# Optimization experiments

Hardware: AMD Instinct MI355X
Metric: run time of the kernel (lower is better)

Reference implementation:

```python
import jax, jax.numpy as jnp
import numpy as np

EMBED_DIM = 1024
NUM_HEADS = 16
HEAD_DIM = EMBED_DIM // NUM_HEADS
SCALE = 1.0 / np.sqrt(HEAD_DIM)


def _quant_linear(x, w, b):
    # Per-tensor symmetric int8 quantize -> dequantize -> GEMM (faithful to QuantizedLinear)
    s = jnp.max(jnp.abs(w)) / 127.0
    w_dq = jnp.clip(jnp.round(w / s), -128.0, 127.0) * s
    return jnp.einsum('bse,oe->bso', x, w_dq) + b


def setup_inputs() -> dict:
    key = jax.random.key(0)
    ks = jax.random.split(key, 7)
    B, S, E = 2, 2048, EMBED_DIM
    return {
        'query': jax.random.normal(ks[0], (B, S, E), dtype=jnp.float32),
        'key': jax.random.normal(ks[1], (B, S, E), dtype=jnp.float32),
        'value': jax.random.normal(ks[2], (B, S, E), dtype=jnp.float32),
        'Wq': jax.random.normal(ks[3], (E, E), dtype=jnp.float32) * 0.02,
        'bq': jnp.zeros((E,), dtype=jnp.float32),
        'Wk': jax.random.normal(ks[4], (E, E), dtype=jnp.float32) * 0.02,
        'bk': jnp.zeros((E,), dtype=jnp.float32),
        'Wv': jax.random.normal(ks[5], (E, E), dtype=jnp.float32) * 0.02,
        'bv': jnp.zeros((E,), dtype=jnp.float32),
        'Wo': jax.random.normal(ks[6], (E, E), dtype=jnp.float32) * 0.02,
        'bo': jnp.zeros((E,), dtype=jnp.float32),
    }


def reference(query, key, value, Wq, bq, Wk, bk, Wv, bv, Wo, bo):
    B, S, E = query.shape
    H, D = NUM_HEADS, HEAD_DIM
    Q = _quant_linear(query, Wq, bq).reshape(B, S, H, D).transpose(0, 2, 1, 3)
    K = _quant_linear(key, Wk, bk).reshape(B, S, H, D).transpose(0, 2, 1, 3)
    V = _quant_linear(value, Wv, bv).reshape(B, S, H, D).transpose(0, 2, 1, 3)
    # [B,H,S,S] unfused attention scores
    scores = jnp.einsum('bhqd,bhkd->bhqk', Q, K) * SCALE
    attn = jax.nn.softmax(scores, axis=-1)  # dropout is identity at inference
    out = jnp.einsum('bhqk,bhkd->bhqd', attn, V)
    out = out.transpose(0, 2, 1, 3).reshape(B, S, E)
    return _quant_linear(out, Wo, bo)
```

## Files before the change

### kernel.cpp

```cpp
#include <hip/hip_runtime.h>
#include <math.h>

#define S_LEN 2048
#define EMB   1024
#define NHEAD 16
#define HDIM  64
#define MTOT  4096
#define EXP2_SCALE 0.18033688011112042f

typedef __attribute__((ext_vector_type(8))) short bf16x8;
typedef __attribute__((ext_vector_type(4))) float f32x4;

__device__ __forceinline__ short f2bf(float f) {
  union { float f; unsigned u; } v; v.f = f;
  unsigned r = v.u + 0x7fffu + ((v.u >> 16) & 1u);
  return (short)(r >> 16);
}
__device__ __forceinline__ float bf2f(short s) {
  union { float f; unsigned u; } v; v.u = ((unsigned)(unsigned short)s) << 16;
  return v.f;
}
__device__ __forceinline__ unsigned pkbf(float e0, float e1) {
  unsigned a = __float_as_uint(e1) + 0x8000u;
  unsigned b = __float_as_uint(e0) + 0x8000u;
  return __builtin_amdgcn_perm(a, b, 0x07060302u);
}

__device__ __forceinline__ void gload_lds16(const void* g, void* l) {
  __builtin_amdgcn_global_load_lds(
      (const __attribute__((address_space(1))) void*)g,
      (__attribute__((address_space(3))) void*)l, 16, 0, 0);
}

__global__ void wabsmax_k(const float* __restrict__ W0, const float* __restrict__ W1,
                          const float* __restrict__ W2, const float* __restrict__ W3,
                          unsigned* __restrict__ scaleU) {
  int w = blockIdx.x & 3;
  int part = blockIdx.x >> 2;
  const float* W = (w == 0) ? W0 : (w == 1) ? W1 : (w == 2) ? W2 : W3;
  float m = 0.f;
  int base = part * 16384;
#pragma unroll
  for (int p = 0; p < 16; ++p) {
    const float4 v = *(const float4*)&W[base + p * 1024 + threadIdx.x * 4];
    m = fmaxf(m, fmaxf(fmaxf(fabsf(v.x), fabsf(v.y)), fmaxf(fabsf(v.z), fabsf(v.w))));
  }
  __shared__ float red[256];
  red[threadIdx.x] = m;
  __syncthreads();
  for (int s = 128; s > 0; s >>= 1) {
    if (threadIdx.x < s) red[threadIdx.x] = fmaxf(red[threadIdx.x], red[threadIdx.x + s]);
    __syncthreads();
  }
  if (threadIdx.x == 0) atomicMax(&scaleU[w], __float_as_uint(red[0]));
}

__global__ void wquant_k(const float* __restrict__ W0, const float* __restrict__ W1,
                         const float* __restrict__ W2, const float* __restrict__ W3,
                         short* __restrict__ Q0, short* __restrict__ Q1,
                         short* __restrict__ Q2, short* __restrict__ Q3,
                         const unsigned* __restrict__ scaleU, float* __restrict__ sVal) {
  int w = blockIdx.y;
  const float* W = (w == 0) ? W0 : (w == 1) ? W1 : (w == 2) ? W2 : W3;
  short* Q = (w == 0) ? Q0 : (w == 1) ? Q1 : (w == 2) ? Q2 : Q3;
  float s = __uint_as_float(scaleU[w]) * (1.0f / 127.0f);
  if (blockIdx.x == 0 && threadIdx.x == 0) sVal[w] = s;
  int idx = (blockIdx.x * 256 + threadIdx.x) * 4;
  float4 v = *(const float4*)&W[idx];
  short4 q;
  q.x = f2bf(fminf(fmaxf(rintf(v.x / s), -128.f), 127.f));
  q.y = f2bf(fminf(fmaxf(rintf(v.y / s), -128.f), 127.f));
  q.z = f2bf(fminf(fmaxf(rintf(v.z / s), -128.f), 127.f));
  q.w = f2bf(fminf(fmaxf(rintf(v.w / s), -128.f), 127.f));
  *(short4*)&Q[idx] = q;
}

__global__ void acast_k(const float* __restrict__ A0, const float* __restrict__ A1,
                        const float* __restrict__ A2,
                        short* __restrict__ H0, short* __restrict__ H1,
                        short* __restrict__ H2) {
  int w = blockIdx.y;
  const float* A = (w == 0) ? A0 : (w == 1) ? A1 : A2;
  short* H = (w == 0) ? H0 : (w == 1) ? H1 : H2;
  int idx = (blockIdx.x * 256 + threadIdx.x) * 4;
  float4 v = *(const float4*)&A[idx];
  short4 h;
  h.x = f2bf(v.x); h.y = f2bf(v.y); h.z = f2bf(v.z); h.w = f2bf(v.w);
  *(short4*)&H[idx] = h;
}

__device__ __forceinline__ void gemm_core(
    const short* __restrict__ Ah, const short* __restrict__ Bq, int m0, int n0,
    short* AhS, short* BsS, f32x4 acc[4][4]) {
  const int tid = threadIdx.x;
  const int lane = tid & 63, wave = tid >> 6;
  const int quad = lane >> 4, l16 = lane & 15;
  const int wm = wave >> 1, wn = wave & 1;

  const int swrow = lane >> 2, swcol = (lane & 3) * 8;
  const short* agh = Ah + (m0 + wave * 32 + swrow) * 1024 + swcol;
  const short* bgp = Bq + (n0 + wave * 32 + swrow) * 1024 + swcol;
  short* sA0 = AhS + wave * 1024;
  short* sB0 = BsS + wave * 1024;

  for (int k0 = 0; k0 < 1024; k0 += 32) {
    __syncthreads();
    gload_lds16(agh + k0,             sA0);
    gload_lds16(agh + 16 * 1024 + k0, sA0 + 512);
    gload_lds16(bgp + k0,             sB0);
    gload_lds16(bgp + 16 * 1024 + k0, sB0 + 512);
    __syncthreads();
    bf16x8 ah[4], bb[4];
#pragma unroll
    for (int mi = 0; mi < 4; ++mi) {
      int row = wm * 64 + mi * 16 + l16;
      ah[mi] = *(const bf16x8*)&AhS[row * 32 + quad * 8];
    }
#pragma unroll
    for (int ni = 0; ni < 4; ++ni) {
      int row = wn * 64 + ni * 16 + l16;
      bb[ni] = *(const bf16x8*)&BsS[row * 32 + quad * 8];
    }
#pragma unroll
    for (int mi = 0; mi < 4; ++mi)
#pragma unroll
      for (int ni = 0; ni < 4; ++ni)
        acc[mi][ni] = __builtin_amdgcn_mfma_f32_16x16x32_bf16(ah[mi], bb[ni], acc[mi][ni], 0, 0, 0);
  }
}

__global__ __launch_bounds__(256, 2) void gemm_qkv(
    const short* __restrict__ QA, const short* __restrict__ KA, const short* __restrict__ VA,
    const short* __restrict__ WqQ, const short* __restrict__ WkQ, const short* __restrict__ WvQ,
    const float* __restrict__ sVal,
    const float* __restrict__ bq, const float* __restrict__ bk, const float* __restrict__ bv,
    short* __restrict__ Qh, short* __restrict__ Kh, short* __restrict__ Vh) {
  __shared__ __align__(16) short AhS[128 * 32];
  __shared__ __align__(16) short BsS[128 * 32];
  const int z = blockIdx.z;
  const short* Ah = (z == 0) ? QA : (z == 1) ? KA : VA;
  const short* Bq = (z == 0) ? WqQ : (z == 1) ? WkQ : WvQ;
  const float* bias = (z == 0) ? bq : (z == 1) ? bk : bv;
  short* oh = (z == 0) ? Qh : (z == 1) ? Kh : Vh;

  const int m0 = blockIdx.y * 128, n0 = blockIdx.x * 128;
  f32x4 acc[4][4];
#pragma unroll
  for (int i = 0; i < 4; ++i)
#pragma unroll
    for (int j = 0; j < 4; ++j) acc[i][j] = (f32x4){0.f, 0.f, 0.f, 0.f};

  gemm_core(Ah, Bq, m0, n0, AhS, BsS, acc);

  const int lane = threadIdx.x & 63, wave = threadIdx.x >> 6;
  const int quad = lane >> 4, l16 = lane & 15;
  const int wm = wave >> 1, wn = wave & 1;
  float s = sVal[z];
  float post = (z == 0) ? EXP2_SCALE : 1.0f;
#pragma unroll
  for (int mi = 0; mi < 4; ++mi) {
#pragma unroll
    for (int ni = 0; ni < 4; ++ni) {
      int rowb = m0 + wm * 64 + mi * 16 + quad * 4;
      int col = n0 + wn * 64 + ni * 16 + l16;
      float bia = bias[col];
      int h = col >> 6, d = col & 63;
      if (z < 2) {
#pragma unroll
        for (int r = 0; r < 4; ++r) {
          float v = (acc[mi][ni][r] * s + bia) * post;
          int row = rowb + r;
          int b = row >> 11, sq = row & 2047;
          oh[((b * 16 + h) * 2048 + sq) * 64 + d] = f2bf(v);
        }
      } else {
        int b = rowb >> 11, sq = rowb & 2047;
        short4 pk;
        pk.x = f2bf(acc[mi][ni][0] * s + bia);
        pk.y = f2bf(acc[mi][ni][1] * s + bia);
        pk.z = f2bf(acc[mi][ni][2] * s + bia);
        pk.w = f2bf(acc[mi][ni][3] * s + bia);
        *(short4*)&oh[((b * 16 + h) * 64 + d) * 2048 + sq] = pk;
      }
    }
  }
}

__global__ __launch_bounds__(256, 2) void gemm_o(
    const short* __restrict__ OAh, const short* __restrict__ OAl,
    const short* __restrict__ WoQ, const float* __restrict__ sPtr,
    const float* __restrict__ bias, float* __restrict__ outF) {
  __shared__ __align__(16) short AhS[128 * 32];
  __shared__ __align__(16) short AlS[128 * 32];
  __shared__ __align__(16) short BsS[64 * 32];
  const int tid = threadIdx.x;
  const int lane = tid & 63, wave = tid >> 6;
  const int quad = lane >> 4, l16 = lane & 15;
  const int m0 = blockIdx.y * 128, n0 = blockIdx.x * 64;

  f32x4 acc[2][4];
#pragma unroll
  for (int i = 0; i < 2; ++i)
#pragma unroll
    for (int j = 0; j < 4; ++j) acc[i][j] = (f32x4){0.f, 0.f, 0.f, 0.f};

  const int swrow = lane >> 2, swcol = (lane & 3) * 8;
  const short* agh = OAh + (m0 + wave * 32 + swrow) * 1024 + swcol;
  const short* agl = OAl + (m0 + wave * 32 + swrow) * 1024 + swcol;
  const short* bgp = WoQ + (n0 + wave * 16 + swrow) * 1024 + swcol;
  short* sA0 = AhS + wave * 1024;
  short* sA1 = AlS + wave * 1024;
  short* sB0 = BsS + wave * 512;

  for (int k0 = 0; k0 < 1024; k0 += 32) {
    __syncthreads();
    gload_lds16(agh + k0,             sA0);
    gload_lds16(agh + 16 * 1024 + k0, sA0 + 512);
    gload_lds16(agl + k0,             sA1);
    gload_lds16(agl + 16 * 1024 + k0, sA1 + 512);
    gload_lds16(bgp + k0,             sB0);
    __syncthreads();
    bf16x8 ah[2], al[2], bb[4];
#pragma unroll
    for (int mi = 0; mi < 2; ++mi) {
      int row = wave * 32 + mi * 16 + l16;
      ah[mi] = *(const bf16x8*)&AhS[row * 32 + quad * 8];
      al[mi] = *(const bf16x8*)&AlS[row * 32 + quad * 8];
    }
#pragma unroll
    for (int ni = 0; ni < 4; ++ni) {
      int row = ni * 16 + l16;
      bb[ni] = *(const bf16x8*)&BsS[row * 32 + quad * 8];
    }
#pragma unroll
    for (int mi = 0; mi < 2; ++mi)
#pragma unroll
      for (int ni = 0; ni < 4; ++ni) {
        acc[mi][ni] = __builtin_amdgcn_mfma_f32_16x16x32_bf16(ah[mi], bb[ni], acc[mi][ni], 0, 0, 0);
        acc[mi][ni] = __builtin_amdgcn_mfma_f32_16x16x32_bf16(al[mi], bb[ni], acc[mi][ni], 0, 0, 0);
      }
  }

  const float s = *sPtr;
#pragma unroll
  for (int mi = 0; mi < 2; ++mi) {
#pragma unroll
    for (int ni = 0; ni < 4; ++ni) {
      int rowb = m0 + wave * 32 + mi * 16 + quad * 4;
      int col = n0 + ni * 16 + l16;
      float bia = bias[col];
#pragma unroll
      for (int r = 0; r < 4; ++r)
        outF[(rowb + r) * 1024 + col] = acc[mi][ni][r] * s + bia;
    }
  }
}

__global__ __launch_bounds__(256, 2) void flash_k(
    const short* __restrict__ Qh, const short* __restrict__ Kh,
    const short* __restrict__ Vh,
    short* __restrict__ Ohi, short* __restrict__ Olo) {
  __shared__ __align__(16) short Khs[64][72];
  __shared__ __align__(16) short Vhs[64][72];

  const int tid = threadIdx.x;
  const int lane = tid & 63, wave = tid >> 6;
  const int quad = lane >> 4, l16 = lane & 15;
  const int bh = blockIdx.y;
  const int b = bh >> 4, h = bh & 15;
  const int q0 = blockIdx.x * 128 + wave * 32;
  const int qkbase = bh * (S_LEN * HDIM);
  const int vbase  = bh * (HDIM * S_LEN);

  bf16x8 qb[2][2];
#pragma unroll
  for (int g = 0; g < 2; ++g) {
    const int qrow = qkbase + (q0 + g * 16 + l16) * HDIM;
    qb[g][0] = *(const bf16x8*)&Qh[qrow + quad * 8];
    qb[g][1] = *(const bf16x8*)&Qh[qrow + 32 + quad * 8];
  }

  f32x4 zero = {0.f, 0.f, 0.f, 0.f};
  f32x4 oacc[2][4];
#pragma unroll
  for (int g = 0; g < 2; ++g)
#pragma unroll
    for (int i = 0; i < 4; ++i) oacc[g][i] = zero;
  float lsum[2] = {0.f, 0.f};

  const int sr = tid >> 2, sc8 = (tid & 3) * 8;
  const int srP = (sr & 32) | (((sr >> 2) & 1) << 4) | (((sr >> 3) & 3) << 2) | (sr & 3);
  const int kgl = qkbase + sr * HDIM + sc8;
  const int vgl = vbase + sr * S_LEN + sc8;

  bf16x8 pk0 = *(const bf16x8*)&Kh[kgl];
  bf16x8 pk1 = *(const bf16x8*)&Kh[kgl + 32];
  bf16x8 pv0 = *(const bf16x8*)&Vh[vgl];
  bf16x8 pv1 = *(const bf16x8*)&Vh[vgl + 32];

  for (int kt = 0; kt < S_LEN; kt += 64) {
    __syncthreads();
    *(bf16x8*)&Khs[srP][sc8]      = pk0;
    *(bf16x8*)&Khs[srP][sc8 + 32] = pk1;
    *(bf16x8*)&Vhs[sr][sc8]       = pv0;
    *(bf16x8*)&Vhs[sr][sc8 + 32]  = pv1;
    __syncthreads();
    if (kt + 64 < S_LEN) {
      int kg = kgl + (kt + 64) * HDIM;
      int vg = vgl + (kt + 64);
      pk0 = *(const bf16x8*)&Kh[kg];
      pk1 = *(const bf16x8*)&Kh[kg + 32];
      pv0 = *(const bf16x8*)&Vh[vg];
      pv1 = *(const bf16x8*)&Vh[vg + 32];
    }
    f32x4 sc[2][4];
#pragma unroll
    for (int nj = 0; nj < 4; ++nj) {
      const int kr = nj * 16 + l16;
      bf16x8 kf0 = *(const bf16x8*)&Khs[kr][quad * 8];
      bf16x8 kf1 = *(const bf16x8*)&Khs[kr][32 + quad * 8];
#pragma unroll
      for (int g = 0; g < 2; ++g) {
        f32x4 sv = zero;
        sv = __builtin_amdgcn_mfma_f32_16x16x32_bf16(kf0, qb[g][0], sv, 0, 0, 0);
        sv = __builtin_amdgcn_mfma_f32_16x16x32_bf16(kf1, qb[g][1], sv, 0, 0, 0);
        sc[g][nj] = sv;
      }
    }
#pragma unroll
    for (int g = 0; g < 2; ++g) {
#pragma unroll
      for (int nj = 0; nj < 4; ++nj)
#pragma unroll
        for (int r = 0; r < 4; ++r)
          sc[g][nj][r] = exp2f(sc[g][nj][r]);
      float psum = 0.f;
#pragma unroll
      for (int nj = 0; nj < 4; ++nj)
        psum += (sc[g][nj][0] + sc[g][nj][1]) + (sc[g][nj][2] + sc[g][nj][3]);
      psum += __shfl_xor(psum, 16);
      psum += __shfl_xor(psum, 32);
      lsum[g] += psum;
    }
    union { bf16x8 v; unsigned u[4]; } P[2][2];
#pragma unroll
    for (int g = 0; g < 2; ++g) {
      P[g][0].u[0] = pkbf(sc[g][0][0], sc[g][0][1]);
      P[g][0].u[1] = pkbf(sc[g][0][2], sc[g][0][3]);
      P[g][0].u[2] = pkbf(sc[g][1][0], sc[g][1][1]);
      P[g][0].u[3] = pkbf(sc[g][1][2], sc[g][1][3]);
      P[g][1].u[0] = pkbf(sc[g][2][0], sc[g][2][1]);
      P[g][1].u[1] = pkbf(sc[g][2][2], sc[g][2][3]);
      P[g][1].u[2] = pkbf(sc[g][3][0], sc[g][3][1]);
      P[g][1].u[3] = pkbf(sc[g][3][2], sc[g][3][3]);
    }
#pragma unroll
    for (int ni = 0; ni < 4; ++ni) {
      int vr = ni * 16 + l16;
      bf16x8 vf0 = *(const bf16x8*)&Vhs[vr][quad * 8];
      bf16x8 vf1 = *(const bf16x8*)&Vhs[vr][32 + quad * 8];
#pragma unroll
      for (int g = 0; g < 2; ++g) {
        oacc[g][ni] = __builtin_amdgcn_mfma_f32_16x16x32_bf16(P[g][0].v, vf0, oacc[g][ni], 0, 0, 0);
        oacc[g][ni] = __builtin_amdgcn_mfma_f32_16x16x32_bf16(P[g][1].v, vf1, oacc[g][ni], 0, 0, 0);
      }
    }
  }
#pragma unroll
  for (int g = 0; g < 2; ++g) {
#pragma unroll
    for (int r = 0; r < 4; ++r) {
      float inv = 1.f / __shfl(lsum[g], quad * 4 + r);
      int row = b * S_LEN + q0 + g * 16 + quad * 4 + r;
#pragma unroll
      for (int ni = 0; ni < 4; ++ni) {
        float v = oacc[g][ni][r] * inv;
        int idx = row * 1024 + h * 64 + ni * 16 + l16;
        short hi = f2bf(v);
        Ohi[idx] = hi;
        Olo[idx] = f2bf(v - bf2f(hi));
      }
    }
  }
}

extern "C" void kernel_launch(void* const* d_in, const int* in_sizes, int n_in,
                              void* d_out, int out_size, void* d_ws, size_t ws_size,
                              hipStream_t stream) {
  const float* query = (const float*)d_in[0];
  const float* key_i = (const float*)d_in[1];
  const float* value = (const float*)d_in[2];
  const float* Wq = (const float*)d_in[3];
  const float* bq = (const float*)d_in[4];
  const float* Wk = (const float*)d_in[5];
  const float* bk = (const float*)d_in[6];
  const float* Wv = (const float*)d_in[7];
  const float* bv = (const float*)d_in[8];
  const float* Wo = (const float*)d_in[9];
  const float* bo = (const float*)d_in[10];
  float* out = (float*)d_out;

  char* w = (char*)d_ws;
  unsigned* scaleU = (unsigned*)w;
  float* sVal = (float*)(w + 256);
  size_t off = 512;
  const size_t SZ_W = 2097152;
  const size_t SZ_A = 8388608;
  short* WqQ = (short*)(w + off); off += SZ_W;
  short* WkQ = (short*)(w + off); off += SZ_W;
  short* WvQ = (short*)(w + off); off += SZ_W;
  short* WoQ = (short*)(w + off); off += SZ_W;
  short* Qa  = (short*)(w + off); off += SZ_A;
  short* Ka  = (short*)(w + off); off += SZ_A;
  short* Va  = (short*)(w + off); off += SZ_A;
  short* Qh  = (short*)(w + off); off += SZ_A;
  short* Kh  = (short*)(w + off); off += SZ_A;
  short* Vh  = (short*)(w + off); off += SZ_A;
  short* Ohi = Qa;
  short* Olo = Ka;

  (void)hipMemsetAsync(scaleU, 0, 16, stream);
  wabsmax_k<<<256, 256, 0, stream>>>(Wq, Wk, Wv, Wo, scaleU);
  wquant_k<<<dim3(1024, 4), 256, 0, stream>>>(Wq, Wk, Wv, Wo, WqQ, WkQ, WvQ, WoQ, scaleU, sVal);
  acast_k<<<dim3(4096, 3), 256, 0, stream>>>(query, key_i, value, Qa, Ka, Va);
  gemm_qkv<<<dim3(8, 32, 3), 256, 0, stream>>>(Qa, Ka, Va, WqQ, WkQ, WvQ, sVal,
                                               bq, bk, bv, Qh, Kh, Vh);
  flash_k<<<dim3(16, 32), 256, 0, stream>>>(Qh, Kh, Vh, Ohi, Olo);
  gemm_o<<<dim3(16, 32), 256, 0, stream>>>(Ohi, Olo, WoQ, sVal + 3, bo, out);
}
```

Baseline: 258.5 us.

## Compute softmax row sums via MFMA with ones, swizzle LDS, use native exp2

The flash attention kernel now accumulates softmax denominators with an extra MFMA against a vector of bf16 ones, replacing the per-tile VALU adds and cross-lane shuffles. The K/V LDS tiles drop their padding and use an XOR swizzle on odd rows instead, and exp2 uses the native hardware builtin when it is available. The aim is to cut VALU and shuffle work in the inner loop and the LDS footprint. The trade-off is that row sums are now taken from bf16-rounded probabilities, which changes numerics slightly.

```diff
diff --git a/kernel.cpp b/kernel.cpp
--- a/kernel.cpp
+++ b/kernel.cpp
@@ -10,6 +10,12 @@
 
 typedef __attribute__((ext_vector_type(8))) short bf16x8;
 typedef __attribute__((ext_vector_type(4))) float f32x4;
+
+#if __has_builtin(__builtin_amdgcn_exp2f)
+#define FEXP2(x) __builtin_amdgcn_exp2f(x)
+#else
+#define FEXP2(x) exp2f(x)
+#endif
 
 __device__ __forceinline__ short f2bf(float f) {
   union { float f; unsigned u; } v; v.f = f;
@@ -260,8 +266,8 @@
     const short* __restrict__ Qh, const short* __restrict__ Kh,
     const short* __restrict__ Vh,
     short* __restrict__ Ohi, short* __restrict__ Olo) {
-  __shared__ __align__(16) short Khs[64][72];
-  __shared__ __align__(16) short Vhs[64][72];
+  __shared__ __align__(16) short Khs[64 * 64];
+  __shared__ __align__(16) short Vhs[64 * 64];
 
   const int tid = threadIdx.x;
   const int lane = tid & 63, wave = tid >> 6;
@@ -286,7 +292,10 @@
   for (int g = 0; g < 2; ++g)
 #pragma unroll
     for (int i = 0; i < 4; ++i) oacc[g][i] = zero;
-  float lsum[2] = {0.f, 0.f};
+  f32x4 sacc[2] = {zero, zero};
+
+  union { bf16x8 v; unsigned u[4]; } ones_;
+  ones_.u[0] = ones_.u[1] = ones_.u[2] = ones_.u[3] = 0x3F803F80u;
 
   const int sr = tid >> 2, sc8 = (tid & 3) * 8;
   const int srP = (sr & 32) | (((sr >> 2) & 1) << 4) | (((sr >> 3) & 3) << 2) | (sr & 3);
@@ -298,12 +307,14 @@
   bf16x8 pv0 = *(const bf16x8*)&Vh[vgl];
   bf16x8 pv1 = *(const bf16x8*)&Vh[vgl + 32];
 
+#define SIDX(row, col) ((row) * 64 + ((col) ^ (((row) & 1) << 5)))
+
   for (int kt = 0; kt < S_LEN; kt += 64) {
     __syncthreads();
-    *(bf16x8*)&Khs[srP][sc8]      = pk0;
-    *(bf16x8*)&Khs[srP][sc8 + 32] = pk1;
-    *(bf16x8*)&Vhs[sr][sc8]       = pv0;
-    *(bf16x8*)&Vhs[sr][sc8 + 32]  = pv1;
+    *(bf16x8*)&Khs[SIDX(srP, sc8)]      = pk0;
+    *(bf16x8*)&Khs[SIDX(srP, sc8 + 32)] = pk1;
+    *(bf16x8*)&Vhs[SIDX(sr, sc8)]       = pv0;
+    *(bf16x8*)&Vhs[SIDX(sr, sc8 + 32)]  = pv1;
     __syncthreads();
     if (kt + 64 < S_LEN) {
       int kg = kgl + (kt + 64) * HDIM;
@@ -317,8 +328,8 @@
 #pragma unroll
     for (int nj = 0; nj < 4; ++nj) {
       const int kr = nj * 16 + l16;
-      bf16x8 kf0 = *(const bf16x8*)&Khs[kr][quad * 8];
-      bf16x8 kf1 = *(const bf16x8*)&Khs[kr][32 + quad * 8];
+      bf16x8 kf0 = *(const bf16x8*)&Khs[SIDX(kr, quad * 8)];
+      bf16x8 kf1 = *(const bf16x8*)&Khs[SIDX(kr, 32 + quad * 8)];
 #pragma unroll
       for (int g = 0; g < 2; ++g) {
         f32x4 sv = zero;
@@ -328,20 +339,12 @@
       }
     }
 #pragma unroll
-    for (int g = 0; g < 2; ++g) {
+    for (int g = 0; g < 2; ++g)
 #pragma unroll
       for (int nj = 0; nj < 4; ++nj)
 #pragma unroll
         for (int r = 0; r < 4; ++r)
-          sc[g][nj][r] = exp2f(sc[g][nj][r]);
-      float psum = 0.f;
-#pragma unroll
-      for (int nj = 0; nj < 4; ++nj)
-        psum += (sc[g][nj][0] + sc[g][nj][1]) + (sc[g][nj][2] + sc[g][nj][3]);
-      psum += __shfl_xor(psum, 16);
-      psum += __shfl_xor(psum, 32);
-      lsum[g] += psum;
-    }
+          sc[g][nj][r] = FEXP2(sc[g][nj][r]);
     union { bf16x8 v; unsigned u[4]; } P[2][2];
 #pragma unroll
     for (int g = 0; g < 2; ++g) {
@@ -355,10 +358,15 @@
       P[g][1].u[3] = pkbf(sc[g][3][2], sc[g][3][3]);
     }
 #pragma unroll
+    for (int g = 0; g < 2; ++g) {
+      sacc[g] = __builtin_amdgcn_mfma_f32_16x16x32_bf16(P[g][0].v, ones_.v, sacc[g], 0, 0, 0);
+      sacc[g] = __builtin_amdgcn_mfma_f32_16x16x32_bf16(P[g][1].v, ones_.v, sacc[g], 0, 0, 0);
+    }
+#pragma unroll
     for (int ni = 0; ni < 4; ++ni) {
       int vr = ni * 16 + l16;
-      bf16x8 vf0 = *(const bf16x8*)&Vhs[vr][quad * 8];
-      bf16x8 vf1 = *(const bf16x8*)&Vhs[vr][32 + quad * 8];
+      bf16x8 vf0 = *(const bf16x8*)&Vhs[SIDX(vr, quad * 8)];
+      bf16x8 vf1 = *(const bf16x8*)&Vhs[SIDX(vr, 32 + quad * 8)];
 #pragma unroll
       for (int g = 0; g < 2; ++g) {
         oacc[g][ni] = __builtin_amdgcn_mfma_f32_16x16x32_bf16(P[g][0].v, vf0, oacc[g][ni], 0, 0, 0);
@@ -366,11 +374,12 @@
       }
     }
   }
+#undef SIDX
 #pragma unroll
   for (int g = 0; g < 2; ++g) {
 #pragma unroll
     for (int r = 0; r < 4; ++r) {
-      float inv = 1.f / __shfl(lsum[g], quad * 4 + r);
+      float inv = 1.f / sacc[g][r];
       int row = b * S_LEN + q0 + g * 16 + quad * 4 + r;
 #pragma unroll
       for (int ni = 0; ni < 4; ++ni) {
```

Result: faster. 244.0 us (-5.6%).
